# Optimization experiments

Hardware: AMD Instinct MI355X
Metric: run time of the kernel (lower is better)

Reference implementation:

```python
import jax, jax.numpy as jnp
import numpy as np

B, N, D = 2, 128, 512  # batch, tokens, embed_dim (= in_features = out_features)
LAYERS = 3


def setup_inputs() -> dict:
    key = jax.random.key(0)
    ks = jax.random.split(key, 9)
    s = lambda fan_in: 1.0 / np.sqrt(fan_in)
    return {
        "text_embedding": jax.random.normal(ks[0], (B, N, D), dtype=jnp.float32),
        # weights stored as [in, out] so y = x @ W + b (matches torch Linear math)
        "W_rel": jax.random.uniform(ks[1], (2 * D, D), jnp.float32, -s(2 * D), s(2 * D)),
        "b_rel": jax.random.uniform(ks[2], (D,), jnp.float32, -s(2 * D), s(2 * D)),
        "W_go": jax.random.uniform(ks[3], (D, D), jnp.float32, -s(D), s(D)),
        "b_go": jax.random.uniform(ks[4], (D,), jnp.float32, -s(D), s(D)),
        "W_gr": jax.random.uniform(ks[5], (3 * D, D), jnp.float32, -s(3 * D), s(3 * D)),
        "b_gr": jax.random.uniform(ks[6], (D,), jnp.float32, -s(3 * D), s(3 * D)),
        "W_esa": jax.random.uniform(ks[7], (D, D), jnp.float32, -s(D), s(D)),
        "b_esa": jax.random.uniform(ks[8], (D,), jnp.float32, -s(D), s(D)),
    }


def reference(text_embedding, W_rel, b_rel, W_go, b_go, W_gr, b_gr, W_esa, b_esa):
    x = text_embedding  # [B, N, D]
    n = x.shape[1]
    rel = None
    for i in range(LAYERS):
        new_x = jnp.tanh(x @ W_go + b_go)  # [B, N, D]
        # pairwise broadcast-concat: [B, N, N, 2D]
        a = jnp.broadcast_to(x[:, :, None, :], (x.shape[0], n, n, x.shape[-1]))
        b = jnp.broadcast_to(x[:, None, :, :], (x.shape[0], n, n, x.shape[-1]))
        rlf = jnp.concatenate([a, b], axis=3)
        if i == 0:
            rel = rlf @ W_rel + b_rel  # [B, N, N, D]
        rlf2 = jnp.concatenate([rlf, rel], axis=3)  # [B, N, N, 3D]
        rel = jnp.tanh(rlf2 @ W_gr + b_gr)  # [B, N, N, D]
        x = new_x
    rel = rel @ W_esa + b_esa  # [B, N, N, D]
    # original subtracts max over dim=1 then applies Softmax(dim=1); equivalent to stable softmax over axis 1
    attn = jax.nn.softmax(rel, axis=1)
    rel_out = jnp.sum(attn * rel, axis=-2)  # sum over second N axis -> [B, N, D]
    return (x, rel_out)
```

## Files before the change

### kernel.cpp

```cpp
#include <hip/hip_runtime.h>
#include <hip/hip_bf16.h>
#include <stdint.h>


#define DEV static __device__ __forceinline__

typedef float  f32x4   __attribute__((ext_vector_type(4)));
typedef float  f32x16  __attribute__((ext_vector_type(16)));
typedef __bf16 bf16x8  __attribute__((ext_vector_type(8)));
typedef __bf16 bf16x4  __attribute__((ext_vector_type(4)));

DEV float tanh_fast(float x) {
  float e = __expf(2.0f * x);
  return 1.0f - 2.0f * __frcp_rn(e + 1.0f);
}

DEV void gl_lds16(const void* g, void* l) {
  __builtin_amdgcn_global_load_lds(
      (const __attribute__((address_space(1))) unsigned int*)g,
      (__attribute__((address_space(3))) unsigned int*)l, 16, 0, 0);
}

struct WC { const float* W; __bf16* Wh; __bf16* Wl; };
struct Prep {
  WC w[7];
  const float* x0; __bf16* x0h; __bf16* x0l;
  const float* b_rel; const float* Wgrc; const float* b_gr; float* dvec;
};

__global__ __launch_bounds__(256) void prep_kernel(Prep pp) {
  const int y = blockIdx.y;
  if (y < 7) {
    const WC wc = pp.w[y];
    __shared__ float tile[32][33];
    int t = threadIdx.x;
    int tx = t & 31, ty = t >> 5;
    int bx = blockIdx.x & 15, by = blockIdx.x >> 4;
    int k0 = by * 32, n0 = bx * 32;
#pragma unroll
    for (int r = 0; r < 4; ++r) {
      int k = ty + r * 8;
      tile[k][tx] = wc.W[(size_t)(k0 + k) * 512 + n0 + tx];
    }
    __syncthreads();
#pragma unroll
    for (int r = 0; r < 4; ++r) {
      int n = ty + r * 8;
      float v = tile[tx][n];
      __bf16 h = (__bf16)v;
      wc.Wh[(size_t)(n0 + n) * 512 + k0 + tx] = h;
      wc.Wl[(size_t)(n0 + n) * 512 + k0 + tx] = (__bf16)(v - (float)h);
    }
  } else if (y == 7) {
    int i = blockIdx.x * 256 + threadIdx.x;
    if (i < 32768) {
      float4 v = ((const float4*)pp.x0)[i];
      float vv[4] = {v.x, v.y, v.z, v.w};
      bf16x4 h, l;
#pragma unroll
      for (int e = 0; e < 4; ++e) {
        __bf16 he = (__bf16)vv[e];
        h[e] = he;
        l[e] = (__bf16)(vv[e] - (float)he);
      }
      ((bf16x4*)pp.x0h)[i] = h;
      ((bf16x4*)pp.x0l)[i] = l;
    }
  } else {
    if (blockIdx.x < 2) {
      int n = blockIdx.x * 256 + threadIdx.x;
      float acc = pp.b_gr[n];
#pragma unroll 8
      for (int k = 0; k < 512; ++k) acc += pp.b_rel[k] * pp.Wgrc[(size_t)k * 512 + n];
      pp.dvec[n] = acc;
    }
  }
}

struct MOp {
  const __bf16* Xh; const __bf16* Xl;
  const __bf16* Wh; const __bf16* Wl;
  const float* bias;
  const float* add;
  float* outf;
  __bf16* outh; __bf16* outl;
  int act;
};
struct MBatch { MOp op[5]; };

__global__ __launch_bounds__(256, 2) void mfma_small_kernel(MBatch batch) {
  const MOp o = batch.op[blockIdx.y];
  const int m0 = ((int)blockIdx.x >> 3) * 64;
  const int n0 = ((int)blockIdx.x & 7) * 64;
  __shared__ __bf16 Ah[64 * 64], Al[64 * 64], Bh[64 * 64], Bl[64 * 64];
  const int t = threadIdx.x, lane = t & 63, wave = t >> 6;
  const int waveM = wave >> 1, waveN = wave & 1;
  const bool comp = (o.Xl != nullptr);

  f32x4 vzero = {0.f, 0.f, 0.f, 0.f};
  f32x4 acc[2][2];
#pragma unroll
  for (int a = 0; a < 2; ++a)
#pragma unroll
    for (int c = 0; c < 2; ++c) acc[a][c] = vzero;

  const int lr = lane >> 3, lc = (lane & 7) * 8;

  for (int k0 = 0; k0 < 512; k0 += 64) {
    __syncthreads();
#pragma unroll
    for (int r = 0; r < 2; ++r) {
      const int rb = r * 32 + wave * 8;
      gl_lds16(o.Xh + (size_t)(m0 + rb + lr) * 512 + k0 + lc, &Ah[rb * 64]);
      gl_lds16(o.Wh + (size_t)(n0 + rb + lr) * 512 + k0 + lc, &Bh[rb * 64]);
      if (comp) {
        gl_lds16(o.Xl + (size_t)(m0 + rb + lr) * 512 + k0 + lc, &Al[rb * 64]);
        gl_lds16(o.Wl + (size_t)(n0 + rb + lr) * 512 + k0 + lc, &Bl[rb * 64]);
      }
    }
    __syncthreads();
#pragma unroll
    for (int kk = 0; kk < 2; ++kk) {
      const int koff = kk * 32 + (lane >> 4) * 8;
      const int ml = lane & 15;
      bf16x8 ah[2], bh[2], al[2], bl[2];
#pragma unroll
      for (int tm = 0; tm < 2; ++tm)
        ah[tm] = *(const bf16x8*)&Ah[(waveM * 32 + tm * 16 + ml) * 64 + koff];
#pragma unroll
      for (int tn = 0; tn < 2; ++tn)
        bh[tn] = *(const bf16x8*)&Bh[(waveN * 32 + tn * 16 + ml) * 64 + koff];
      if (comp) {
#pragma unroll
        for (int tm = 0; tm < 2; ++tm)
          al[tm] = *(const bf16x8*)&Al[(waveM * 32 + tm * 16 + ml) * 64 + koff];
#pragma unroll
        for (int tn = 0; tn < 2; ++tn)
          bl[tn] = *(const bf16x8*)&Bl[(waveN * 32 + tn * 16 + ml) * 64 + koff];
      }
#pragma unroll
      for (int tm = 0; tm < 2; ++tm)
#pragma unroll
        for (int tn = 0; tn < 2; ++tn) {
          acc[tm][tn] = __builtin_amdgcn_mfma_f32_16x16x32_bf16(ah[tm], bh[tn], acc[tm][tn], 0, 0, 0);
          if (comp) {
            acc[tm][tn] = __builtin_amdgcn_mfma_f32_16x16x32_bf16(ah[tm], bl[tn], acc[tm][tn], 0, 0, 0);
            acc[tm][tn] = __builtin_amdgcn_mfma_f32_16x16x32_bf16(al[tm], bh[tn], acc[tm][tn], 0, 0, 0);
          }
        }
    }
  }

  const int quad = lane >> 4, cl = lane & 15;
#pragma unroll
  for (int tm = 0; tm < 2; ++tm) {
#pragma unroll
    for (int r = 0; r < 4; ++r) {
      const int row = m0 + waveM * 32 + tm * 16 + quad * 4 + r;
#pragma unroll
      for (int tn = 0; tn < 2; ++tn) {
        const int col = n0 + waveN * 32 + tn * 16 + cl;
        float v = acc[tm][tn][r];
        if (o.bias) v += o.bias[col];
        if (o.add) v += o.add[(size_t)row * 512 + col];
        if (o.act) v = tanh_fast(v);
        if (o.outf) o.outf[(size_t)row * 512 + col] = v;
        if (o.outh) {
          __bf16 h = (__bf16)v;
          o.outh[(size_t)row * 512 + col] = h;
          o.outl[(size_t)row * 512 + col] = (__bf16)(v - (float)h);
        }
      }
    }
  }
}

__global__ __launch_bounds__(256) void rel1_kernel(
    const float* __restrict__ A, const float* __restrict__ C,
    __bf16* __restrict__ R1) {
  size_t e = ((size_t)blockIdx.x * 256 + threadIdx.x) * 8;
  int d = (int)(e & 511);
  int j = (int)((e >> 9) & 127);
  int bi = (int)(e >> 16);
  int b = bi >> 7;
  const float* ap = &A[(size_t)bi * 512 + d];
  const float* cp = &C[((size_t)(b * 128 + j)) * 512 + d];
  float av[8], cv[8];
  *(float4*)&av[0] = *(const float4*)ap;
  *(float4*)&av[4] = *(const float4*)(ap + 4);
  *(float4*)&cv[0] = *(const float4*)cp;
  *(float4*)&cv[4] = *(const float4*)(cp + 4);
  bf16x8 o;
#pragma unroll
  for (int k = 0; k < 8; ++k) o[k] = (__bf16)tanh_fast(av[k] + cv[k]);
  *(bf16x8*)&R1[e] = o;
}

constexpr int BM = 128, BN = 128, BK = 64;
DEV int lds_off(int row) { return row * 64 + (row >> 3) * 8; }

template <int MODE>
__global__ __launch_bounds__(256, 2) void big_gemm_kernel(
    const __bf16* __restrict__ Ab, const __bf16* __restrict__ Wt,
    const float* __restrict__ P, const float* __restrict__ Q,
    const float* __restrict__ bias, __bf16* __restrict__ outb,
    float* __restrict__ outf) {
  __shared__ __bf16 As[BM * BK + 16 * 8];
  __shared__ __bf16 Bs[BN * BK + 16 * 8];
  const int t = threadIdx.x;
  const int lane = t & 63;
  const int wave = t >> 6;
  const int bm = (int)blockIdx.x >> 2;
  const int n0 = ((int)blockIdx.x & 3) * BN;
  const size_t r0 = (size_t)bm * BM;
  const int b = bm >> 7;
  const int i = bm & 127;
  const int waveM = wave >> 1, waveN = wave & 1;

  f32x16 acc[2][2];
#pragma unroll
  for (int a = 0; a < 2; ++a)
#pragma unroll
    for (int c = 0; c < 2; ++c) acc[a][c] = (f32x16)0.f;

  for (int k0 = 0; k0 < 512; k0 += BK) {
    __syncthreads();
#pragma unroll
    for (int p2 = 0; p2 < 4; ++p2) {
      int rowg = wave * 32 + p2 * 8;
      const __bf16* ga = Ab + (r0 + rowg + (lane >> 3)) * 512 + k0 + (lane & 7) * 8;
      gl_lds16(ga, &As[lds_off(rowg)]);
      const __bf16* gb = Wt + (size_t)(n0 + rowg + (lane >> 3)) * 512 + k0 + (lane & 7) * 8;
      gl_lds16(gb, &Bs[lds_off(rowg)]);
    }
    __syncthreads();
    const int ml = lane & 31;
    const int kl = (lane >> 5) * 8;
#pragma unroll
    for (int ks = 0; ks < 4; ++ks) {
      const int koff = ks * 16 + kl;
      bf16x8 af[2], bfr[2];
#pragma unroll
      for (int tm = 0; tm < 2; ++tm)
        af[tm] = *(const bf16x8*)&As[lds_off(waveM * 64 + tm * 32 + ml) + koff];
#pragma unroll
      for (int tn = 0; tn < 2; ++tn)
        bfr[tn] = *(const bf16x8*)&Bs[lds_off(waveN * 64 + tn * 32 + ml) + koff];
#pragma unroll
      for (int tm = 0; tm < 2; ++tm)
#pragma unroll
        for (int tn = 0; tn < 2; ++tn)
          acc[tm][tn] = __builtin_amdgcn_mfma_f32_32x32x16_bf16(af[tm], bfr[tn], acc[tm][tn], 0, 0, 0);
    }
  }

  const int cl = lane & 31, lg = lane >> 5;
#pragma unroll
  for (int tm = 0; tm < 2; ++tm) {
#pragma unroll
    for (int tn = 0; tn < 2; ++tn) {
      const int col = n0 + waveN * 64 + tn * 32 + cl;
      float pv;
      if (MODE == 2) pv = bias[col];
      else pv = P[((size_t)(b * 128 + i)) * 512 + col];
#pragma unroll
      for (int reg = 0; reg < 16; ++reg) {
        const int row = waveM * 64 + tm * 32 + (reg & 3) + 8 * (reg >> 2) + 4 * lg;
        float v = acc[tm][tn][reg] + pv;
        if (MODE == 2) {
          outf[(r0 + row) * 512 + col] = v;
        } else {
          v += Q[((size_t)(b * 128 + row)) * 512 + col];
          outb[(r0 + row) * 512 + col] = (__bf16)tanh_fast(v);
        }
      }
    }
  }
}

__global__ __launch_bounds__(256) void softmax_l_kernel(
    const float* __restrict__ S, float* __restrict__ Lb) {
  int idx = blockIdx.x * 256 + threadIdx.x;
  int d = idx & 511;
  int j = (idx >> 9) & 127;
  int b = idx >> 16;
  const float* p = S + ((size_t)b * 16384 + j) * 512 + d;
  float l = 0.f;
#pragma unroll 8
  for (int ii = 0; ii < 128; ++ii) l += __expf(p[(size_t)ii * 65536]);
  Lb[idx] = __frcp_rn(l);
}

__global__ __launch_bounds__(256) void softmax_out_kernel(
    const float* __restrict__ S, const float* __restrict__ Lb,
    float* __restrict__ outp) {
  int idx = blockIdx.x * 256 + threadIdx.x;
  int d = idx & 511;
  int i = (idx >> 9) & 127;
  int b = idx >> 16;
  const float* sp = S + ((size_t)(b * 128 + i)) * 65536 + d;
  const float* lp = Lb + (size_t)b * 65536 + d;
  float acc = 0.f;
#pragma unroll 8
  for (int jj = 0; jj < 128; ++jj) {
    float s = sp[(size_t)jj * 512];
    acc += __expf(s) * lp[(size_t)jj * 512] * s;
  }
  outp[idx] = acc;
}

extern "C" void kernel_launch(void* const* d_in, const int* in_sizes, int n_in,
                              void* d_out, int out_size, void* d_ws, size_t ws_size,
                              hipStream_t stream) {
  const float* x0    = (const float*)d_in[0];
  const float* W_rel = (const float*)d_in[1];
  const float* b_rel = (const float*)d_in[2];
  const float* W_go  = (const float*)d_in[3];
  const float* b_go  = (const float*)d_in[4];
  const float* W_gr  = (const float*)d_in[5];
  const float* b_gr  = (const float*)d_in[6];
  const float* W_esa = (const float*)d_in[7];
  const float* b_esa = (const float*)d_in[8];

  const float* Wrel_top = W_rel;
  const float* Wrel_bot = W_rel + 512 * 512;
  const float* Wgr_a = W_gr;
  const float* Wgr_b = W_gr + 512 * 512;
  const float* Wgr_c = W_gr + 2 * 512 * 512;

  char* ws = (char*)d_ws;
  size_t off = 0;
  auto alloc = [&](size_t bytes) -> void* {
    void* p = ws + off;
    off += (bytes + 255) & ~(size_t)255;
    return p;
  };
  const size_t NREL = 16777216ull;
  float*  S  = (float*)alloc(NREL * 4);
  __bf16* R1 = (__bf16*)alloc(NREL * 2);
  __bf16* R2 = (__bf16*)alloc(NREL * 2);
  float* p0t  = (float*)alloc(131072 * 4);
  float* q0t  = (float*)alloc(131072 * 4);
  float* Abuf = (float*)alloc(131072 * 4);
  float* Cbuf = (float*)alloc(131072 * 4);
  float* p1   = (float*)alloc(131072 * 4);
  float* q1   = (float*)alloc(131072 * 4);
  float* p2   = (float*)alloc(131072 * 4);
  float* q2   = (float*)alloc(131072 * 4);
  float* dvec = (float*)alloc(512 * 4);
  float* Lb   = (float*)alloc(131072 * 4);
  __bf16* x0h = (__bf16*)alloc(131072 * 2);
  __bf16* x0l = (__bf16*)alloc(131072 * 2);
  __bf16* x1h = (__bf16*)alloc(131072 * 2);
  __bf16* x1l = (__bf16*)alloc(131072 * 2);
  __bf16* x2h = (__bf16*)alloc(131072 * 2);
  __bf16* x2l = (__bf16*)alloc(131072 * 2);
  __bf16* u0h = (__bf16*)alloc(131072 * 2);
  __bf16* u0l = (__bf16*)alloc(131072 * 2);
  __bf16* v0h = (__bf16*)alloc(131072 * 2);
  __bf16* v0l = (__bf16*)alloc(131072 * 2);
  __bf16* Wgo_h = (__bf16*)alloc(262144 * 2);
  __bf16* Wgo_l = (__bf16*)alloc(262144 * 2);
  __bf16* Wrt_h = (__bf16*)alloc(262144 * 2);
  __bf16* Wrt_l = (__bf16*)alloc(262144 * 2);
  __bf16* Wrb_h = (__bf16*)alloc(262144 * 2);
  __bf16* Wrb_l = (__bf16*)alloc(262144 * 2);
  __bf16* Wga_h = (__bf16*)alloc(262144 * 2);
  __bf16* Wga_l = (__bf16*)alloc(262144 * 2);
  __bf16* Wgb_h = (__bf16*)alloc(262144 * 2);
  __bf16* Wgb_l = (__bf16*)alloc(262144 * 2);
  __bf16* Wgc_h = (__bf16*)alloc(262144 * 2);
  __bf16* Wgc_l = (__bf16*)alloc(262144 * 2);
  __bf16* Wes_h = (__bf16*)alloc(262144 * 2);
  __bf16* Wes_l = (__bf16*)alloc(262144 * 2);

  float* x3out  = (float*)d_out;
  float* relout = (float*)d_out + 131072;

  Prep pp;
  pp.w[0] = {W_go, Wgo_h, Wgo_l};
  pp.w[1] = {Wrel_top, Wrt_h, Wrt_l};
  pp.w[2] = {Wrel_bot, Wrb_h, Wrb_l};
  pp.w[3] = {Wgr_a, Wga_h, Wga_l};
  pp.w[4] = {Wgr_b, Wgb_h, Wgb_l};
  pp.w[5] = {Wgr_c, Wgc_h, Wgc_l};
  pp.w[6] = {W_esa, Wes_h, Wes_l};
  pp.x0 = x0; pp.x0h = x0h; pp.x0l = x0l;
  pp.b_rel = b_rel; pp.Wgrc = Wgr_c; pp.b_gr = b_gr; pp.dvec = dvec;
  prep_kernel<<<dim3(256, 9), 256, 0, stream>>>(pp);

  MBatch m1 = {};
  m1.op[0] = {x0h, x0l, Wgo_h, Wgo_l, b_go, nullptr, nullptr, x1h, x1l, 1};
  m1.op[1] = {x0h, x0l, Wrt_h, Wrt_l, nullptr, nullptr, nullptr, u0h, u0l, 0};
  m1.op[2] = {x0h, x0l, Wrb_h, Wrb_l, nullptr, nullptr, nullptr, v0h, v0l, 0};
  m1.op[3] = {x0h, x0l, Wga_h, Wga_l, nullptr, nullptr, p0t, nullptr, nullptr, 0};
  m1.op[4] = {x0h, x0l, Wgb_h, Wgb_l, nullptr, nullptr, q0t, nullptr, nullptr, 0};
  mfma_small_kernel<<<dim3(32, 5), 256, 0, stream>>>(m1);

  MBatch m2 = {};
  m2.op[0] = {x1h, x1l, Wgo_h, Wgo_l, b_go, nullptr, nullptr, x2h, x2l, 1};
  m2.op[1] = {u0h, u0l, Wgc_h, Wgc_l, dvec, p0t, Abuf, nullptr, nullptr, 0};
  m2.op[2] = {v0h, v0l, Wgc_h, Wgc_l, nullptr, q0t, Cbuf, nullptr, nullptr, 0};
  m2.op[3] = {x1h, x1l, Wga_h, Wga_l, b_gr, nullptr, p1, nullptr, nullptr, 0};
  m2.op[4] = {x1h, x1l, Wgb_h, Wgb_l, nullptr, nullptr, q1, nullptr, nullptr, 0};
  mfma_small_kernel<<<dim3(32, 5), 256, 0, stream>>>(m2);

  MBatch m3 = {};
  m3.op[0] = {x2h, x2l, Wgo_h, Wgo_l, b_go, nullptr, x3out, nullptr, nullptr, 1};
  m3.op[1] = {x2h, x2l, Wga_h, Wga_l, b_gr, nullptr, p2, nullptr, nullptr, 0};
  m3.op[2] = {x2h, x2l, Wgb_h, Wgb_l, nullptr, nullptr, q2, nullptr, nullptr, 0};
  mfma_small_kernel<<<dim3(32, 3), 256, 0, stream>>>(m3);

  rel1_kernel<<<8192, 256, 0, stream>>>(Abuf, Cbuf, R1);

  big_gemm_kernel<1><<<1024, 256, 0, stream>>>(R1, Wgc_h, p1, q1, nullptr, R2, nullptr);
  big_gemm_kernel<1><<<1024, 256, 0, stream>>>(R2, Wgc_h, p2, q2, nullptr, R1, nullptr);
  big_gemm_kernel<2><<<1024, 256, 0, stream>>>(R1, Wes_h, nullptr, nullptr, b_esa, nullptr, S);

  softmax_l_kernel<<<512, 256, 0, stream>>>(S, Lb);
  softmax_out_kernel<<<512, 256, 0, stream>>>(S, Lb, relout);
}
```

Before: 269.5 us.

## Fuse rel init and three chained rel GEMMs into one LDS-resident kernel

```diff
diff --git a/kernel.cpp b/kernel.cpp
--- a/kernel.cpp
+++ b/kernel.cpp
@@ -175,107 +175,105 @@
   }
 }
 
-__global__ __launch_bounds__(256) void rel1_kernel(
-    const float* __restrict__ A, const float* __restrict__ C,
-    __bf16* __restrict__ R1) {
-  size_t e = ((size_t)blockIdx.x * 256 + threadIdx.x) * 8;
-  int d = (int)(e & 511);
-  int j = (int)((e >> 9) & 127);
-  int bi = (int)(e >> 16);
-  int b = bi >> 7;
-  const float* ap = &A[(size_t)bi * 512 + d];
-  const float* cp = &C[((size_t)(b * 128 + j)) * 512 + d];
-  float av[8], cv[8];
-  *(float4*)&av[0] = *(const float4*)ap;
-  *(float4*)&av[4] = *(const float4*)(ap + 4);
-  *(float4*)&cv[0] = *(const float4*)cp;
-  *(float4*)&cv[4] = *(const float4*)(cp + 4);
-  bf16x8 o;
-#pragma unroll
-  for (int k = 0; k < 8; ++k) o[k] = (__bf16)tanh_fast(av[k] + cv[k]);
-  *(bf16x8*)&R1[e] = o;
-}
-
-constexpr int BM = 128, BN = 128, BK = 64;
-DEV int lds_off(int row) { return row * 64 + (row >> 3) * 8; }
-
-template <int MODE>
-__global__ __launch_bounds__(256, 2) void big_gemm_kernel(
-    const __bf16* __restrict__ Ab, const __bf16* __restrict__ Wt,
-    const float* __restrict__ P, const float* __restrict__ Q,
-    const float* __restrict__ bias, __bf16* __restrict__ outb,
-    float* __restrict__ outf) {
-  __shared__ __bf16 As[BM * BK + 16 * 8];
-  __shared__ __bf16 Bs[BN * BK + 16 * 8];
-  const int t = threadIdx.x;
-  const int lane = t & 63;
-  const int wave = t >> 6;
-  const int bm = (int)blockIdx.x >> 2;
-  const int n0 = ((int)blockIdx.x & 3) * BN;
-  const size_t r0 = (size_t)bm * BM;
-  const int b = bm >> 7;
-  const int i = bm & 127;
-  const int waveM = wave >> 1, waveN = wave & 1;
-
-  f32x16 acc[2][2];
-#pragma unroll
-  for (int a = 0; a < 2; ++a)
-#pragma unroll
-    for (int c = 0; c < 2; ++c) acc[a][c] = (f32x16)0.f;
-
-  for (int k0 = 0; k0 < 512; k0 += BK) {
-    __syncthreads();
-#pragma unroll
-    for (int p2 = 0; p2 < 4; ++p2) {
-      int rowg = wave * 32 + p2 * 8;
-      const __bf16* ga = Ab + (r0 + rowg + (lane >> 3)) * 512 + k0 + (lane & 7) * 8;
-      gl_lds16(ga, &As[lds_off(rowg)]);
-      const __bf16* gb = Wt + (size_t)(n0 + rowg + (lane >> 3)) * 512 + k0 + (lane & 7) * 8;
-      gl_lds16(gb, &Bs[lds_off(rowg)]);
-    }
-    __syncthreads();
-    const int ml = lane & 31;
-    const int kl = (lane >> 5) * 8;
-#pragma unroll
-    for (int ks = 0; ks < 4; ++ks) {
-      const int koff = ks * 16 + kl;
-      bf16x8 af[2], bfr[2];
-#pragma unroll
-      for (int tm = 0; tm < 2; ++tm)
-        af[tm] = *(const bf16x8*)&As[lds_off(waveM * 64 + tm * 32 + ml) + koff];
-#pragma unroll
-      for (int tn = 0; tn < 2; ++tn)
-        bfr[tn] = *(const bf16x8*)&Bs[lds_off(waveN * 64 + tn * 32 + ml) + koff];
-#pragma unroll
-      for (int tm = 0; tm < 2; ++tm)
-#pragma unroll
-        for (int tn = 0; tn < 2; ++tn)
-          acc[tm][tn] = __builtin_amdgcn_mfma_f32_32x32x16_bf16(af[tm], bfr[tn], acc[tm][tn], 0, 0, 0);
-    }
-  }
+DEV int p_byte(int row, int col ) {
+  return row * 1024 + ((col * 2) ^ ((row & 15) << 4));
+}
+
+template <bool FINAL>
+DEV void chain_stage(__bf16* P, const __bf16* __restrict__ Wt,
+                     const float* __restrict__ pv,
+                     const float* __restrict__ qv,
+                     float* __restrict__ Sout,
+                     int lane, int wave) {
+  const int ml = lane & 31, kl = lane >> 5;
+  f32x16 acc[2][4];
+#pragma unroll
+  for (int tm = 0; tm < 2; ++tm)
+#pragma unroll
+    for (int tn = 0; tn < 4; ++tn) acc[tm][tn] = (f32x16)0.f;
+
+  const __bf16* wbase = Wt + (size_t)(wave * 128 + ml) * 512 + kl * 8;
+#pragma unroll 4
+  for (int ks = 0; ks < 32; ++ks) {
+    bf16x8 af[2], bfr[4];
+#pragma unroll
+    for (int tn = 0; tn < 4; ++tn)
+      bfr[tn] = *(const bf16x8*)&wbase[(size_t)(tn * 32) * 512 + ks * 16];
+#pragma unroll
+    for (int tm = 0; tm < 2; ++tm)
+      af[tm] = *(const bf16x8*)((const char*)P + p_byte(tm * 32 + ml, ks * 16 + kl * 8));
+#pragma unroll
+    for (int tm = 0; tm < 2; ++tm)
+#pragma unroll
+      for (int tn = 0; tn < 4; ++tn)
+        acc[tm][tn] = __builtin_amdgcn_mfma_f32_32x32x16_bf16(af[tm], bfr[tn], acc[tm][tn], 0, 0, 0);
+  }
+
+  __syncthreads();
 
   const int cl = lane & 31, lg = lane >> 5;
 #pragma unroll
-  for (int tm = 0; tm < 2; ++tm) {
-#pragma unroll
-    for (int tn = 0; tn < 2; ++tn) {
-      const int col = n0 + waveN * 64 + tn * 32 + cl;
-      float pv;
-      if (MODE == 2) pv = bias[col];
-      else pv = P[((size_t)(b * 128 + i)) * 512 + col];
+  for (int tm = 0; tm < 2; ++tm)
+#pragma unroll
+    for (int tn = 0; tn < 4; ++tn) {
+      const int col = wave * 128 + tn * 32 + cl;
+      const float pval = pv[col];
 #pragma unroll
       for (int reg = 0; reg < 16; ++reg) {
-        const int row = waveM * 64 + tm * 32 + (reg & 3) + 8 * (reg >> 2) + 4 * lg;
-        float v = acc[tm][tn][reg] + pv;
-        if (MODE == 2) {
-          outf[(r0 + row) * 512 + col] = v;
+        const int row = tm * 32 + (reg & 3) + 8 * (reg >> 2) + 4 * lg;
+        float v = acc[tm][tn][reg] + pval;
+        if constexpr (FINAL) {
+          Sout[(size_t)row * 512 + col] = v;
         } else {
-          v += Q[((size_t)(b * 128 + row)) * 512 + col];
-          outb[(r0 + row) * 512 + col] = (__bf16)tanh_fast(v);
+          v += qv[(size_t)row * 512 + col];
+          *(__bf16*)((char*)P + p_byte(row, col)) = (__bf16)tanh_fast(v);
         }
       }
     }
-  }
+  if constexpr (!FINAL) __syncthreads();
+}
+
+__global__ __launch_bounds__(256, 2) void chain_kernel(
+    const float* __restrict__ A, const float* __restrict__ C,
+    const __bf16* __restrict__ Wgc, const __bf16* __restrict__ Wes,
+    const float* __restrict__ p1, const float* __restrict__ q1,
+    const float* __restrict__ p2, const float* __restrict__ q2,
+    const float* __restrict__ b_esa, float* __restrict__ S) {
+  __shared__ __bf16 P[64 * 512];
+  const int t = threadIdx.x, lane = t & 63, wave = t >> 6;
+  const int blk = blockIdx.x;
+  const size_t r0 = (size_t)blk * 64;
+  const int bi = blk >> 1;
+  const int b = bi >> 7;
+  const int j0 = (blk & 1) * 64;
+
+  {
+    const float* arow = A + (size_t)bi * 512;
+#pragma unroll
+    for (int c = 0; c < 16; ++c) {
+      int chunk = c * 256 + t;
+      int row = chunk >> 6;
+      int col = (chunk & 63) * 8;
+      const float* ap = arow + col;
+      const float* cp = C + ((size_t)(b * 128 + j0 + row)) * 512 + col;
+      float av[8], cv[8];
+      *(float4*)&av[0] = *(const float4*)ap;
+      *(float4*)&av[4] = *(const float4*)(ap + 4);
+      *(float4*)&cv[0] = *(const float4*)cp;
+      *(float4*)&cv[4] = *(const float4*)(cp + 4);
+      bf16x8 o;
+#pragma unroll
+      for (int e = 0; e < 8; ++e) o[e] = (__bf16)tanh_fast(av[e] + cv[e]);
+      *(bf16x8*)((char*)P + p_byte(row, col)) = o;
+    }
+  }
+  __syncthreads();
+
+  chain_stage<false>(P, Wgc, p1 + (size_t)bi * 512,
+                     q1 + ((size_t)(b * 128 + j0)) * 512, nullptr, lane, wave);
+  chain_stage<false>(P, Wgc, p2 + (size_t)bi * 512,
+                     q2 + ((size_t)(b * 128 + j0)) * 512, nullptr, lane, wave);
+  chain_stage<true>(P, Wes, b_esa, nullptr, S + r0 * 512, lane, wave);
 }
 
 __global__ __launch_bounds__(256) void softmax_l_kernel(
@@ -337,8 +335,6 @@
   };
   const size_t NREL = 16777216ull;
   float*  S  = (float*)alloc(NREL * 4);
-  __bf16* R1 = (__bf16*)alloc(NREL * 2);
-  __bf16* R2 = (__bf16*)alloc(NREL * 2);
   float* p0t  = (float*)alloc(131072 * 4);
   float* q0t  = (float*)alloc(131072 * 4);
   float* Abuf = (float*)alloc(131072 * 4);
@@ -411,11 +407,8 @@
   m3.op[2] = {x2h, x2l, Wgb_h, Wgb_l, nullptr, nullptr, q2, nullptr, nullptr, 0};
   mfma_small_kernel<<<dim3(32, 3), 256, 0, stream>>>(m3);
 
-  rel1_kernel<<<8192, 256, 0, stream>>>(Abuf, Cbuf, R1);
-
-  big_gemm_kernel<1><<<1024, 256, 0, stream>>>(R1, Wgc_h, p1, q1, nullptr, R2, nullptr);
-  big_gemm_kernel<1><<<1024, 256, 0, stream>>>(R2, Wgc_h, p2, q2, nullptr, R1, nullptr);
-  big_gemm_kernel<2><<<1024, 256, 0, stream>>>(R1, Wes_h, nullptr, nullptr, b_esa, nullptr, S);
+  chain_kernel<<<512, 256, 0, stream>>>(Abuf, Cbuf, Wgc_h, Wes_h,
+                                        p1, q1, p2, q2, b_esa, S);
 
   softmax_l_kernel<<<512, 256, 0, stream>>>(S, Lb);
   softmax_out_kernel<<<512, 256, 0, stream>>>(S, Lb, relout);
```

Result: slower. 407.1 us (+51.1%).
